# Optimization experiments

Measured on AMD Instinct MI355X. Metric: run time of the kernel, lower is better.

The kernel has to match this reference:

```python
import jax, jax.numpy as jnp
import numpy as np
from jax import lax

SOBEL_X = jnp.array([[-1., 0., 1.], [-2., 0., 2.], [-1., 0., 1.]], jnp.float32)
SCHARR_X = jnp.array([[-3., 0., 3.], [-10., 0., 10.], [-3., 0., 3.]], jnp.float32)

# year routing map baked in (configure()): 2019->sobel(0), 2020->scharr(1), default learnable(2)

def _dwconv(x, k2d):
    """Depthwise 3x3 conv with the same 2D kernel per channel, padding=1."""
    C = x.shape[1]
    kern = jnp.broadcast_to(k2d, (C, 1, 3, 3))
    return lax.conv_general_dilated(
        x, kern, window_strides=(1, 1), padding='SAME',
        dimension_numbers=('NCHW', 'OIHW', 'NCHW'), feature_group_count=C)


def _edge_mag(x, kx, ky, eps):
    gx = _dwconv(x, kx)
    gy = _dwconv(x, ky)
    return jnp.sqrt(gx * gx + gy * gy + eps)


def setup_inputs() -> dict:
    key = jax.random.key(0)
    k1, k2 = jax.random.split(key)
    x = jax.random.normal(k1, (32, 9, 256, 256), jnp.float32)
    year = 2018 + jax.random.randint(k2, (32,), 0, 4)  # years 2018..2021
    alpha = jnp.asarray(0.5, jnp.float32)
    scale = jnp.ones((1,), jnp.float32) * 0.1
    return {"x": x, "alpha": alpha, "scale": scale, "year": year}


def reference(x, alpha, scale, year):
    B = x.shape[0]
    # fixed operators
    sobel_out = _edge_mag(x, SOBEL_X, SOBEL_X.T, 1e-8)
    scharr_out = _edge_mag(x, SCHARR_X, SCHARR_X.T, 1e-8)
    # learnable operator: sigmoid-mixed kernel, normalized by max abs
    a = jax.nn.sigmoid(alpha)
    kx = a * SOBEL_X + (1.0 - a) * SCHARR_X
    kx = kx / jnp.max(jnp.abs(kx))
    ky = kx.T  # sobel_y = sobel_x.T and scharr_y = scharr_x.T, mix commutes with transpose
    learnable_out = _edge_mag(x, kx, ky, 1e-6) * jax.nn.sigmoid(scale)
    # per-sample routing: 2019 -> sobel, 2020 -> scharr, else default learnable
    op_idx = jnp.where(year == 2019, 0, jnp.where(year == 2020, 1, 2))
    stacked = jnp.stack([sobel_out, scharr_out, learnable_out])  # [3,B,C,H,W]
    mixed = stacked[op_idx, jnp.arange(B)]
    return mixed
```

## Files before the change

kernel.cpp:

```cpp
#include <hip/hip_runtime.h>
#include <math.h>

#define BATCH 32
#define CHANS 9
#define HH 256
#define WW 256
#define RPW 4

typedef float f32x4 __attribute__((ext_vector_type(4)));

__global__ __launch_bounds__(256) void edge_router_kernel(
    const float* __restrict__ x,
    const float* __restrict__ alpha_p,
    const float* __restrict__ scale_p,
    const int*   __restrict__ year,
    float* __restrict__ out)
{
    const int tid  = threadIdx.x;
    const int lane = tid & 63;

    const int nblk = (BATCH * CHANS * (HH / RPW)) / 4;
    const int bpc  = nblk >> 3;
    const int bid  = blockIdx.x;
    const int sbid = (bid & 7) * bpc + (bid >> 3);

    const int gwave = sbid * 4 + (tid >> 6);
    const int rb    = gwave & (HH / RPW - 1);
    const int plane = gwave >> 6;
    const int b     = plane / CHANS;
    const int r0    = rb * RPW;
    const int xq    = lane * 4;

    const float* __restrict__ p = x   + (size_t)plane * (HH * WW) + xq;
    float*       __restrict__ q = out + (size_t)plane * (HH * WW) + xq;

    f32x4 rows[RPW + 2];
#pragma unroll
    for (int i = 0; i < RPW + 2; ++i) {
        int y = r0 - 1 + i;
        y = y < 0 ? 0 : (y > HH - 1 ? HH - 1 : y);
        rows[i] = *reinterpret_cast<const f32x4*>(p + (size_t)y * WW);
    }
    if (r0 == 0)        rows[0]       = (f32x4)0.f;
    if (r0 == HH - RPW) rows[RPW + 1] = (f32x4)0.f;

    const int yr = year[b];
    float w0, w1, eps, post;
    if (yr == 2019) {
        w0 = 1.f; w1 = 2.f; eps = 1e-8f; post = 1.f;
    } else if (yr == 2020) {
        w0 = 3.f; w1 = 10.f; eps = 1e-8f; post = 1.f;
    } else {
        const float a = 1.f / (1.f + expf(-alpha_p[0]));
        const float m = 10.f - 8.f * a;
        w0 = (3.f - 2.f * a) / m;
        w1 = 1.f;
        eps = 1e-6f;
        post = 1.f / (1.f + expf(-scale_p[0]));
    }

    auto finish_row = [&](f32x4 t, f32x4 u, int y) {
        float tl = __shfl_up(t.w, 1);
        float ul = __shfl_up(u.w, 1);
        if (lane == 0)  { tl = 0.f; ul = 0.f; }
        float tr = __shfl_down(t.x, 1);
        float ur = __shfl_down(u.x, 1);
        if (lane == 63) { tr = 0.f; ur = 0.f; }

        f32x4 gx, gy;
        gx.x = t.y - tl;   gx.y = t.z - t.x;
        gx.z = t.w - t.y;  gx.w = tr - t.z;
        gy.x = fmaf(w1, u.x, w0 * (ul + u.y));
        gy.y = fmaf(w1, u.y, w0 * (u.x + u.z));
        gy.z = fmaf(w1, u.z, w0 * (u.y + u.w));
        gy.w = fmaf(w1, u.w, w0 * (u.z + ur));

        f32x4 o;
        o.x = sqrtf(fmaf(gx.x, gx.x, fmaf(gy.x, gy.x, eps))) * post;
        o.y = sqrtf(fmaf(gx.y, gx.y, fmaf(gy.y, gy.y, eps))) * post;
        o.z = sqrtf(fmaf(gx.z, gx.z, fmaf(gy.z, gy.z, eps))) * post;
        o.w = sqrtf(fmaf(gx.w, gx.w, fmaf(gy.w, gy.w, eps))) * post;

        *reinterpret_cast<f32x4*>(q + (size_t)y * WW) = o;
    };

#pragma unroll
    for (int i = 0; i < RPW; ++i) {
        const f32x4 va = rows[i];
        const f32x4 vb = rows[i + 1];
        const f32x4 vc = rows[i + 2];
        f32x4 t, u;
        t.x = fmaf(w1, vb.x, w0 * (va.x + vc.x));
        t.y = fmaf(w1, vb.y, w0 * (va.y + vc.y));
        t.z = fmaf(w1, vb.z, w0 * (va.z + vc.z));
        t.w = fmaf(w1, vb.w, w0 * (va.w + vc.w));
        u = vc - va;
        finish_row(t, u, r0 + i);
    }
}

extern "C" void kernel_launch(void* const* d_in, const int* in_sizes, int n_in,
                              void* d_out, int out_size, void* d_ws, size_t ws_size,
                              hipStream_t stream) {
    const float* x     = (const float*)d_in[0];
    const float* alpha = (const float*)d_in[1];
    const float* scale = (const float*)d_in[2];
    const int*   year  = (const int*)  d_in[3];
    float* out = (float*)d_out;

    const int waves  = BATCH * CHANS * (HH / RPW);
    const int blocks = waves / 4;
    edge_router_kernel<<<blocks, 256, 0, stream>>>(x, alpha, scale, year, out);
}
```

Before: 135.5 us.

## Stage 16-row strips in LDS via direct global-to-LDS loads, share halo rows

Each block now covers a 16-row strip of one plane. It loads 18 rows into shared memory with direct global-to-LDS loads, and each wave then reads its 6 rows from LDS. Before, every wave loaded its own 6 rows from global memory, so halo rows were read twice; now only 18 of them are read per 16 output rows. The change also drops the XCD-aware block swizzle and switches to the hardware sqrt builtin. The costs are a block barrier, LDS traffic, and possibly slightly different sqrt rounding.

```diff
diff --git a/kernel.cpp b/kernel.cpp
--- a/kernel.cpp
+++ b/kernel.cpp
@@ -5,9 +5,20 @@
 #define CHANS 9
 #define HH 256
 #define WW 256
-#define RPW 4
+#define SROWS 16
+#define LROWS (SROWS + 2)
 
 typedef float f32x4 __attribute__((ext_vector_type(4)));
+typedef const __attribute__((address_space(1))) void* gas_ptr;
+typedef __attribute__((address_space(3))) void* las_ptr;
+
+static __device__ __forceinline__ float fast_sqrtf(float v) {
+#if __has_builtin(__builtin_amdgcn_sqrtf)
+    return __builtin_amdgcn_sqrtf(v);
+#else
+    return sqrtf(v);
+#endif
+}
 
 __global__ __launch_bounds__(256) void edge_router_kernel(
     const float* __restrict__ x,
@@ -16,33 +27,30 @@
     const int*   __restrict__ year,
     float* __restrict__ out)
 {
+    __shared__ float lds[LROWS][WW];
+
     const int tid  = threadIdx.x;
     const int lane = tid & 63;
+    const int w    = tid >> 6;
 
-    const int nblk = (BATCH * CHANS * (HH / RPW)) / 4;
-    const int bpc  = nblk >> 3;
-    const int bid  = blockIdx.x;
-    const int sbid = (bid & 7) * bpc + (bid >> 3);
-
-    const int gwave = sbid * 4 + (tid >> 6);
-    const int rb    = gwave & (HH / RPW - 1);
-    const int plane = gwave >> 6;
+    const int strip = blockIdx.x & (HH / SROWS - 1);
+    const int plane = blockIdx.x >> 4;
     const int b     = plane / CHANS;
-    const int r0    = rb * RPW;
+    const int r0    = strip * SROWS;
     const int xq    = lane * 4;
 
-    const float* __restrict__ p = x   + (size_t)plane * (HH * WW) + xq;
+    const float* __restrict__ p = x   + (size_t)plane * (HH * WW);
     float*       __restrict__ q = out + (size_t)plane * (HH * WW) + xq;
 
-    f32x4 rows[RPW + 2];
+    auto load_row = [&](int l) {
+        int y = r0 - 1 + l;
+        y = y < 0 ? 0 : (y > HH - 1 ? HH - 1 : y);
+        const float* g = p + (size_t)y * WW + xq;
+        __builtin_amdgcn_global_load_lds((gas_ptr)g, (las_ptr)&lds[l][0], 16, 0, 0);
+    };
 #pragma unroll
-    for (int i = 0; i < RPW + 2; ++i) {
-        int y = r0 - 1 + i;
-        y = y < 0 ? 0 : (y > HH - 1 ? HH - 1 : y);
-        rows[i] = *reinterpret_cast<const f32x4*>(p + (size_t)y * WW);
-    }
-    if (r0 == 0)        rows[0]       = (f32x4)0.f;
-    if (r0 == HH - RPW) rows[RPW + 1] = (f32x4)0.f;
+    for (int k = 0; k < 4; ++k) load_row(w + 4 * k);
+    if (w < 2) load_row(w + 16);
 
     const int yr = year[b];
     float w0, w1, eps, post;
@@ -58,6 +66,16 @@
         eps = 1e-6f;
         post = 1.f / (1.f + expf(-scale_p[0]));
     }
+
+    __syncthreads();
+
+    const int R0 = r0 + 4 * w;
+    f32x4 v[6];
+#pragma unroll
+    for (int j = 0; j < 6; ++j)
+        v[j] = *reinterpret_cast<const f32x4*>(&lds[4 * w + j][xq]);
+    if (R0 == 0)           v[0] = (f32x4)0.f;
+    if (R0 + 3 == HH - 1)  v[5] = (f32x4)0.f;
 
     auto finish_row = [&](f32x4 t, f32x4 u, int y) {
         float tl = __shfl_up(t.w, 1);
@@ -76,26 +94,26 @@
         gy.w = fmaf(w1, u.w, w0 * (u.z + ur));
 
         f32x4 o;
-        o.x = sqrtf(fmaf(gx.x, gx.x, fmaf(gy.x, gy.x, eps))) * post;
-        o.y = sqrtf(fmaf(gx.y, gx.y, fmaf(gy.y, gy.y, eps))) * post;
-        o.z = sqrtf(fmaf(gx.z, gx.z, fmaf(gy.z, gy.z, eps))) * post;
-        o.w = sqrtf(fmaf(gx.w, gx.w, fmaf(gy.w, gy.w, eps))) * post;
+        o.x = fast_sqrtf(fmaf(gx.x, gx.x, fmaf(gy.x, gy.x, eps))) * post;
+        o.y = fast_sqrtf(fmaf(gx.y, gx.y, fmaf(gy.y, gy.y, eps))) * post;
+        o.z = fast_sqrtf(fmaf(gx.z, gx.z, fmaf(gy.z, gy.z, eps))) * post;
+        o.w = fast_sqrtf(fmaf(gx.w, gx.w, fmaf(gy.w, gy.w, eps))) * post;
 
         *reinterpret_cast<f32x4*>(q + (size_t)y * WW) = o;
     };
 
 #pragma unroll
-    for (int i = 0; i < RPW; ++i) {
-        const f32x4 va = rows[i];
-        const f32x4 vb = rows[i + 1];
-        const f32x4 vc = rows[i + 2];
+    for (int i = 0; i < 4; ++i) {
+        const f32x4 va = v[i];
+        const f32x4 vb = v[i + 1];
+        const f32x4 vc = v[i + 2];
         f32x4 t, u;
         t.x = fmaf(w1, vb.x, w0 * (va.x + vc.x));
         t.y = fmaf(w1, vb.y, w0 * (va.y + vc.y));
         t.z = fmaf(w1, vb.z, w0 * (va.z + vc.z));
         t.w = fmaf(w1, vb.w, w0 * (va.w + vc.w));
         u = vc - va;
-        finish_row(t, u, r0 + i);
+        finish_row(t, u, R0 + i);
     }
 }
 
@@ -108,7 +126,6 @@
     const int*   year  = (const int*)  d_in[3];
     float* out = (float*)d_out;
 
-    const int waves  = BATCH * CHANS * (HH / RPW);
-    const int blocks = waves / 4;
+    const int blocks = BATCH * CHANS * (HH / SROWS);
     edge_router_kernel<<<blocks, 256, 0, stream>>>(x, alpha, scale, year, out);
 }
```

New measurement: 135.4 us. No clear change (-0.1%).
